# Kernel optimization log

Hardware: AMD Instinct MI355X
Metric: run time of the kernel (lower is better)

## Reference

```python
import jax, jax.numpy as jnp
import numpy as np

N_NODES = 100000
N_EDGES = 3200000
IN_DIM, HID, OUT = 256, 64, 10


def setup_inputs() -> dict:
    key = jax.random.key(0)
    ks = jax.random.split(key, 6)
    x = jax.random.normal(ks[0], (N_NODES, IN_DIM), jnp.float32)
    edge_index = jax.random.randint(ks[1], (2, N_EDGES), 0, N_NODES, dtype=jnp.int64)
    edge_weight = jnp.ones((N_EDGES,), jnp.float32)
    # Glorot-scaled weights; PyG GCNConv keeps bias separate from lin.
    W1 = jax.random.normal(ks[2], (HID, IN_DIM), jnp.float32) * np.float32(1.0 / np.sqrt(IN_DIM))
    b1 = jnp.zeros((HID,), jnp.float32)
    W2 = jax.random.normal(ks[3], (HID, HID), jnp.float32) * np.float32(1.0 / np.sqrt(HID))
    b2 = jnp.zeros((HID,), jnp.float32)
    W3 = jax.random.normal(ks[4], (OUT, HID), jnp.float32) * np.float32(1.0 / np.sqrt(HID))
    b3 = jnp.zeros((OUT,), jnp.float32)
    return dict(x=x, edge_index=edge_index, edge_weight=edge_weight,
                W1=W1, b1=b1, W2=W2, b2=b2, W3=W3, b3=b3)


def _gcn_conv(x, W, b, row, col, edge_weight, n):
    """PyG GCNConv with add_self_loops=False: out = D^{-1/2} A D^{-1/2} (x W^T) + b."""
    h = x @ W.T  # [N, out_dim]
    deg = jax.ops.segment_sum(edge_weight, col, num_segments=n)  # in-degree by weight
    dinv = jnp.where(deg > 0, jax.lax.rsqrt(jnp.maximum(deg, 1e-12)), 0.0)
    norm = dinv[row] * edge_weight * dinv[col]  # [E]
    msgs = h[row] * norm[:, None]               # gather from source nodes
    out = jax.ops.segment_sum(msgs, col, num_segments=n)  # scatter-add to targets
    return out + b


def reference(x, edge_index, edge_weight, W1, b1, W2, b2, W3, b3):
    row, col = edge_index[0], edge_index[1]
    n = x.shape[0]
    h = jax.nn.relu(_gcn_conv(x, W1, b1, row, col, edge_weight, n))
    h = jax.nn.relu(_gcn_conv(h, W2, b2, row, col, edge_weight, n))
    out = _gcn_conv(h, W3, b3, row, col, edge_weight, n)  # logits, [N, num_classes]
    return out
```

## Files before the change

### kernel.cpp

```cpp
#include <hip/hip_runtime.h>
#include <stddef.h>

typedef __attribute__((ext_vector_type(8))) short bf16x8;
typedef __attribute__((ext_vector_type(4))) float f32x4;
typedef __attribute__((ext_vector_type(8))) float f32x8;

#define NPB 512
#define PB  512

__device__ inline float bf2f(unsigned short u) {
    unsigned int v = ((unsigned int)u) << 16;
    float f;
    __builtin_memcpy(&f, &v, 4);
    return f;
}
__device__ inline unsigned short f2bf(float f) {
    unsigned int v;
    __builtin_memcpy(&v, &f, 4);
    unsigned int r = (v + 0x7FFFu + ((v >> 16) & 1u)) >> 16;
    return (unsigned short)r;
}
__device__ inline float feat(const void* p, long long idx, int isbf) {
    if (isbf) return bf2f(((const unsigned short*)p)[idx]);
    return ((const float*)p)[idx];
}
__device__ inline int clampi(int v, int lo, int hi) {
    return v < lo ? lo : (v > hi ? hi : v);
}

__global__ void detect_kernel(const int* ei, const unsigned short* ew16,
                              const unsigned short* x16, int* flags) {
    __shared__ int s_is64, s_pass;
    if (threadIdx.x == 0) { s_is64 = 1; s_pass = 0; }
    __syncthreads();
    int t = threadIdx.x;
    if (t < 128 && ei[2 * t + 1] != 0) atomicAnd(&s_is64, 0);
    if (t < 64) {
        unsigned short h = x16[t];
        unsigned int expf = (h >> 7) & 0xFF;
        if (h == 0 || (expf >= 112 && expf <= 142)) atomicAdd(&s_pass, 1);
    }
    __syncthreads();
    if (t == 0) {
        flags[0] = s_is64;
        flags[1] = (ew16[0] == 0x3F80) ? 1 : 0;
        flags[2] = (s_pass >= 56) ? 1 : 0;
        flags[3] = 1;
    }
}

__global__ void ones_kernel(const void* ew, int* flags, int E) {
    int i = blockIdx.x * blockDim.x + threadIdx.x;
    int wbf = flags[1];
    int b = i * 4;
    int lim = b + 4 < E ? b + 4 : E;
    bool bad = false;
    for (int k = b; k < lim; k++)
        if (feat(ew, k, wbf) != 1.0f) bad = true;
    if (bad) atomicAnd(&flags[3], 0);
}

__global__ void sentinel_kernel(unsigned short* outp, int n, float val) {
    int i = blockIdx.x * blockDim.x + threadIdx.x;
    if (i < n) outp[i] = f2bf(val);
}

__global__ void wsplit_kernel(const void* W, const int* flags, unsigned short* hi,
                              unsigned short* lo, int n_in, int n_out) {
    int i = blockIdx.x * blockDim.x + threadIdx.x;
    if (i >= n_out) return;
    if (i >= n_in) { hi[i] = 0; lo[i] = 0; return; }
    if (flags[2]) {
        hi[i] = ((const unsigned short*)W)[i];
        lo[i] = 0;
    } else {
        float v = ((const float*)W)[i];
        unsigned short h = f2bf(v);
        hi[i] = h;
        lo[i] = f2bf(v - bf2f(h));
    }
}

__global__ __launch_bounds__(512) void khist_kernel(const int* ei, const int* flags,
                                                    int* ghist, int E, int n,
                                                    int NB, int chunk) {
    __shared__ int hist[256];
    int blk = blockIdx.x;
    for (int i = threadIdx.x; i < NB; i += blockDim.x) hist[i] = 0;
    __syncthreads();
    int is64 = flags[0];
    int e0 = blk * chunk;
    int e1 = e0 + chunk < E ? e0 + chunk : E;
    for (int e = e0 + (int)threadIdx.x; e < e1; e += blockDim.x) {
        int c = is64 ? ei[2 * (E + e)] : ei[E + e];
        c = clampi(c, 0, n - 1);
        atomicAdd(&hist[c >> 9], 1);
    }
    __syncthreads();
    for (int i = threadIdx.x; i < NB; i += blockDim.x) ghist[blk * NB + i] = hist[i];
}

__global__ __launch_bounds__(512) void koff1_kernel(int* ghist, int* btot, int NB) {
    __shared__ int s[512];
    int b = blockIdx.x;
    int t = threadIdx.x;
    int v = ghist[t * NB + b];
    s[t] = v;
    __syncthreads();
    for (int off = 1; off < 512; off <<= 1) {
        int add = (t >= off) ? s[t - off] : 0;
        __syncthreads();
        s[t] += add;
        __syncthreads();
    }
    ghist[t * NB + b] = s[t] - v;
    if (t == 511) btot[b] = s[511];
}

__global__ __launch_bounds__(256) void koff2_kernel(const int* btot, int* bstart,
                                                    int* row_ptr, int NB, int N, int E) {
    __shared__ int s[256];
    int t = threadIdx.x;
    int v = (t < NB) ? btot[t] : 0;
    s[t] = v;
    __syncthreads();
    for (int off = 1; off < 256; off <<= 1) {
        int add = (t >= off) ? s[t - off] : 0;
        __syncthreads();
        s[t] += add;
        __syncthreads();
    }
    if (t < NB) bstart[t] = s[t] - v;
    if (t == 0) row_ptr[N] = E;
}

__global__ __launch_bounds__(512) void kscatter_kernel(const int* ei, const void* ew,
                                                       const int* flags, const int* ghist,
                                                       const int* bstart,
                                                       unsigned int* ebuf, float* wbuf,
                                                       int E, int n, int NB, int chunk) {
    __shared__ int cur[256];
    int blk = blockIdx.x;
    for (int i = threadIdx.x; i < NB; i += blockDim.x)
        cur[i] = ghist[blk * NB + i] + bstart[i];
    __syncthreads();
    int is64 = flags[0], wbf = flags[1], ones = flags[3];
    int e0 = blk * chunk;
    int e1 = e0 + chunk < E ? e0 + chunk : E;
    for (int e = e0 + (int)threadIdx.x; e < e1; e += blockDim.x) {
        int r = is64 ? ei[2 * e] : ei[e];
        int c = is64 ? ei[2 * (E + e)] : ei[E + e];
        r = clampi(r, 0, n - 1);
        c = clampi(c, 0, n - 1);
        int b = c >> 9;
        int pos = atomicAdd(&cur[b], 1);
        ebuf[pos] = ((unsigned int)(c & 511) << 17) | (unsigned int)r;
        if (!ones) wbuf[pos] = feat(ew, e, wbf);
    }
}

__global__ __launch_bounds__(512) void kcsr_a_kernel(const unsigned int* ebuf,
                                                     const float* wbuf, const int* flags,
                                                     const int* bstart, const int* btot,
                                                     int* row_ptr, float* dinv, int N) {
    __shared__ int cnt[512];
    __shared__ int pre[512];
    __shared__ float wsum[512];
    int b = blockIdx.x;
    int t = threadIdx.x;
    int ones = flags[3];
    cnt[t] = 0;
    wsum[t] = 0.f;
    __syncthreads();
    int bs = bstart[b];
    int be = bs + btot[b];
    for (int i = bs + t; i < be; i += 512) {
        unsigned int p = ebuf[i];
        int cl = (int)(p >> 17);
        atomicAdd(&cnt[cl], 1);
        if (!ones) atomicAdd(&wsum[cl], wbuf[i]);
    }
    __syncthreads();
    int v = cnt[t];
    pre[t] = v;
    __syncthreads();
    for (int off = 1; off < 512; off <<= 1) {
        int add = (t >= off) ? pre[t - off] : 0;
        __syncthreads();
        pre[t] += add;
        __syncthreads();
    }
    int node = b * NPB + t;
    if (node < N) {
        row_ptr[node] = bs + pre[t] - v;
        float d = ones ? (float)v : wsum[t];
        dinv[node] = (d > 0.f) ? rsqrtf(fmaxf(d, 1e-12f)) : 0.f;
    }
}

__global__ __launch_bounds__(512) void kcsr_b_kernel(const unsigned int* ebuf,
                                                     const float* wbuf, const int* flags,
                                                     const int* bstart, const int* btot,
                                                     const int* row_ptr, const float* dinv,
                                                     int2* csr_pack, int N) {
    __shared__ int cur[512];
    __shared__ float dloc[512];
    int b = blockIdx.x;
    int t = threadIdx.x;
    int ones = flags[3];
    int node = b * NPB + t;
    cur[t] = (node < N) ? row_ptr[node] : 0;
    dloc[t] = (node < N) ? dinv[node] : 0.f;
    __syncthreads();
    int bs = bstart[b];
    int be = bs + btot[b];
    for (int i = bs + t; i < be; i += 512) {
        unsigned int p = ebuf[i];
        int cl = (int)(p >> 17);
        int r = (int)(p & 0x1FFFFu);
        float w = ones ? 1.0f : wbuf[i];
        float nv = dinv[r] * w * dloc[cl];
        int pos = atomicAdd(&cur[cl], 1);
        csr_pack[pos] = make_int2(r, __float_as_int(nv));
    }
}

__device__ inline void split8v(f32x8 v, bf16x8& hi, bf16x8& lo) {
    for (int i = 0; i < 8; i++) {
        float f = v[i];
        unsigned short h = f2bf(f);
        hi[i] = (short)h;
        lo[i] = (short)f2bf(f - bf2f(h));
    }
}

__global__ __launch_bounds__(256) void gemm1_kernel(const void* A,
                             const unsigned short* Whi, const unsigned short* Wlo,
                             const int* flags, unsigned short* C, int M, int K) {
    int wave = threadIdx.x >> 6;
    int l = threadIdx.x & 63;
    int m = l & 15;
    int quad = l >> 4;
    int row0 = blockIdx.x * 64 + wave * 16;
    bool arow_ok = (row0 + m) < M;
    int fb = flags[2];
    f32x4 acc[4];
    #pragma unroll
    for (int n = 0; n < 4; n++) acc[n] = (f32x4){0.f, 0.f, 0.f, 0.f};
    bf16x8 zf = {0, 0, 0, 0, 0, 0, 0, 0};
    long long abase = (long long)(row0 + m) * K + quad * 8;
    if (fb) {
        const short* As = (const short*)A;
        #pragma unroll 4
        for (int k0 = 0; k0 < K; k0 += 32) {
            bf16x8 a = arow_ok ? *(const bf16x8*)(As + abase + k0) : zf;
            #pragma unroll
            for (int n = 0; n < 4; n++) {
                const unsigned short* wp = Whi + (long long)(n * 16 + m) * K + k0 + quad * 8;
                bf16x8 b = *(const bf16x8*)wp;
                acc[n] = __builtin_amdgcn_mfma_f32_16x16x32_bf16(a, b, acc[n], 0, 0, 0);
            }
        }
    } else {
        const float* Af = (const float*)A;
        #pragma unroll 2
        for (int k0 = 0; k0 < K; k0 += 32) {
            bf16x8 ah = zf, al = zf;
            if (arow_ok) {
                f32x8 av = *(const f32x8*)(Af + abase + k0);
                split8v(av, ah, al);
            }
            #pragma unroll
            for (int n = 0; n < 4; n++) {
                long long widx = (long long)(n * 16 + m) * K + k0 + quad * 8;
                bf16x8 wh = *(const bf16x8*)(Whi + widx);
                bf16x8 wl = *(const bf16x8*)(Wlo + widx);
                acc[n] = __builtin_amdgcn_mfma_f32_16x16x32_bf16(ah, wh, acc[n], 0, 0, 0);
                acc[n] = __builtin_amdgcn_mfma_f32_16x16x32_bf16(al, wh, acc[n], 0, 0, 0);
                acc[n] = __builtin_amdgcn_mfma_f32_16x16x32_bf16(ah, wl, acc[n], 0, 0, 0);
            }
        }
    }
    #pragma unroll
    for (int n = 0; n < 4; n++) {
        #pragma unroll
        for (int r = 0; r < 4; r++) {
            int row = row0 + quad * 4 + r;
            if (row < M) C[(long long)row * 64 + n * 16 + m] = f2bf(acc[n][r]);
        }
    }
}

__global__ __launch_bounds__(256) void gemm2_kernel(const unsigned short* A,
                             const unsigned short* Whi, const unsigned short* Wlo,
                             const int* flags, unsigned short* C, int M) {
    int wave = threadIdx.x >> 6;
    int l = threadIdx.x & 63;
    int m = l & 15;
    int quad = l >> 4;
    int row0 = blockIdx.x * 64 + wave * 16;
    bool arow_ok = (row0 + m) < M;
    int fb = flags[2];
    f32x4 acc[4];
    #pragma unroll
    for (int n = 0; n < 4; n++) acc[n] = (f32x4){0.f, 0.f, 0.f, 0.f};
    bf16x8 zf = {0, 0, 0, 0, 0, 0, 0, 0};
    const short* As = (const short*)A;
    long long abase = (long long)(row0 + m) * 64 + quad * 8;
    #pragma unroll
    for (int k0 = 0; k0 < 64; k0 += 32) {
        bf16x8 a = arow_ok ? *(const bf16x8*)(As + abase + k0) : zf;
        #pragma unroll
        for (int n = 0; n < 4; n++) {
            long long widx = (long long)(n * 16 + m) * 64 + k0 + quad * 8;
            bf16x8 wh = *(const bf16x8*)(Whi + widx);
            acc[n] = __builtin_amdgcn_mfma_f32_16x16x32_bf16(a, wh, acc[n], 0, 0, 0);
            if (!fb) {
                bf16x8 wl = *(const bf16x8*)(Wlo + widx);
                acc[n] = __builtin_amdgcn_mfma_f32_16x16x32_bf16(a, wl, acc[n], 0, 0, 0);
            }
        }
    }
    #pragma unroll
    for (int n = 0; n < 4; n++) {
        #pragma unroll
        for (int r = 0; r < 4; r++) {
            int row = row0 + quad * 4 + r;
            if (row < M) C[(long long)row * 64 + n * 16 + m] = f2bf(acc[n][r]);
        }
    }
}

__global__ __launch_bounds__(256) void gemm3_kernel(const unsigned short* A,
                             const unsigned short* Whi, const unsigned short* Wlo,
                             const int* flags, unsigned short* C, int M) {
    int wave = threadIdx.x >> 6;
    int l = threadIdx.x & 63;
    int m = l & 15;
    int quad = l >> 4;
    int row0 = blockIdx.x * 64 + wave * 16;
    bool arow_ok = (row0 + m) < M;
    int fb = flags[2];
    f32x4 acc = {0.f, 0.f, 0.f, 0.f};
    bf16x8 zf = {0, 0, 0, 0, 0, 0, 0, 0};
    const short* As = (const short*)A;
    long long abase = (long long)(row0 + m) * 64 + quad * 8;
    #pragma unroll
    for (int k0 = 0; k0 < 64; k0 += 32) {
        bf16x8 a = arow_ok ? *(const bf16x8*)(As + abase + k0) : zf;
        long long widx = (long long)m * 64 + k0 + quad * 8;
        bf16x8 wh = *(const bf16x8*)(Whi + widx);
        acc = __builtin_amdgcn_mfma_f32_16x16x32_bf16(a, wh, acc, 0, 0, 0);
        if (!fb) {
            bf16x8 wl = *(const bf16x8*)(Wlo + widx);
            acc = __builtin_amdgcn_mfma_f32_16x16x32_bf16(a, wl, acc, 0, 0, 0);
        }
    }
    #pragma unroll
    for (int r = 0; r < 4; r++) {
        int row = row0 + quad * 4 + r;
        if (row < M) C[(long long)row * 16 + m] = f2bf(acc[r]);
    }
}

__global__ void agg64_kernel(const unsigned short* h, const void* bias,
                             const int* flags, const int* row_ptr,
                             const int2* cp, unsigned short* outp, int n, int do_relu) {
    int l = threadIdx.x & 63;
    int node = blockIdx.x * 4 + (int)(threadIdx.x >> 6);
    if (node >= n) return;
    int g = l >> 3;
    int j = l & 7;
    int beg = row_ptr[node];
    int end = row_ptr[node + 1];
    float a0 = 0.f, a1 = 0.f, a2 = 0.f, a3 = 0.f;
    float a4 = 0.f, a5 = 0.f, a6 = 0.f, a7 = 0.f;
    for (int e = beg; e < end; e += 8) {
        int ee = e + g;
        if (ee < end) {
            int2 p = cp[ee];
            float nv = __int_as_float(p.y);
            uint4 raw = *(const uint4*)(h + (long long)p.x * 64 + j * 8);
            a0 += nv * __uint_as_float(raw.x << 16);
            a1 += nv * __uint_as_float(raw.x & 0xFFFF0000u);
            a2 += nv * __uint_as_float(raw.y << 16);
            a3 += nv * __uint_as_float(raw.y & 0xFFFF0000u);
            a4 += nv * __uint_as_float(raw.z << 16);
            a5 += nv * __uint_as_float(raw.z & 0xFFFF0000u);
            a6 += nv * __uint_as_float(raw.w << 16);
            a7 += nv * __uint_as_float(raw.w & 0xFFFF0000u);
        }
    }
    for (int mask = 8; mask <= 32; mask <<= 1) {
        a0 += __shfl_xor(a0, mask);
        a1 += __shfl_xor(a1, mask);
        a2 += __shfl_xor(a2, mask);
        a3 += __shfl_xor(a3, mask);
        a4 += __shfl_xor(a4, mask);
        a5 += __shfl_xor(a5, mask);
        a6 += __shfl_xor(a6, mask);
        a7 += __shfl_xor(a7, mask);
    }
    if (g == 0) {
        int fb = flags[2];
        float v0 = a0 + feat(bias, j * 8 + 0, fb);
        float v1 = a1 + feat(bias, j * 8 + 1, fb);
        float v2 = a2 + feat(bias, j * 8 + 2, fb);
        float v3 = a3 + feat(bias, j * 8 + 3, fb);
        float v4 = a4 + feat(bias, j * 8 + 4, fb);
        float v5 = a5 + feat(bias, j * 8 + 5, fb);
        float v6 = a6 + feat(bias, j * 8 + 6, fb);
        float v7 = a7 + feat(bias, j * 8 + 7, fb);
        if (do_relu) {
            v0 = fmaxf(v0, 0.f); v1 = fmaxf(v1, 0.f);
            v2 = fmaxf(v2, 0.f); v3 = fmaxf(v3, 0.f);
            v4 = fmaxf(v4, 0.f); v5 = fmaxf(v5, 0.f);
            v6 = fmaxf(v6, 0.f); v7 = fmaxf(v7, 0.f);
        }
        uint4 pk;
        pk.x = (unsigned int)f2bf(v0) | ((unsigned int)f2bf(v1) << 16);
        pk.y = (unsigned int)f2bf(v2) | ((unsigned int)f2bf(v3) << 16);
        pk.z = (unsigned int)f2bf(v4) | ((unsigned int)f2bf(v5) << 16);
        pk.w = (unsigned int)f2bf(v6) | ((unsigned int)f2bf(v7) << 16);
        *(uint4*)(outp + (long long)node * 64 + j * 8) = pk;
    }
}

__global__ void agg16_kernel(const unsigned short* h, const void* bias,
                             const int* flags, const int* row_ptr,
                             const int2* cp, void* outp, int n) {
    int l = threadIdx.x & 63;
    int node = blockIdx.x * 4 + (int)(threadIdx.x >> 6);
    if (node >= n) return;
    int g = l >> 2;
    int j = l & 3;
    int beg = row_ptr[node];
    int end = row_ptr[node + 1];
    float a0 = 0.f, a1 = 0.f, a2 = 0.f, a3 = 0.f;
    for (int e = beg; e < end; e += 16) {
        int ee = e + g;
        if (ee < end) {
            int2 p = cp[ee];
            float nv = __int_as_float(p.y);
            uint2 raw = *(const uint2*)(h + (long long)p.x * 16 + j * 4);
            a0 += nv * __uint_as_float(raw.x << 16);
            a1 += nv * __uint_as_float(raw.x & 0xFFFF0000u);
            a2 += nv * __uint_as_float(raw.y << 16);
            a3 += nv * __uint_as_float(raw.y & 0xFFFF0000u);
        }
    }
    for (int mask = 4; mask <= 32; mask <<= 1) {
        a0 += __shfl_xor(a0, mask);
        a1 += __shfl_xor(a1, mask);
        a2 += __shfl_xor(a2, mask);
        a3 += __shfl_xor(a3, mask);
    }
    if (g == 0) {
        int fb = flags[2];
        float v[4] = {a0, a1, a2, a3};
        #pragma unroll
        for (int i = 0; i < 4; i++) {
            int f = j * 4 + i;
            if (f < 10) {
                float o = v[i] + feat(bias, f, fb);
                if (fb) ((unsigned short*)outp)[(long long)node * 10 + f] = f2bf(o);
                else    ((float*)outp)[(long long)node * 10 + f] = o;
            }
        }
    }
}

extern "C" void kernel_launch(void* const* d_in, const int* in_sizes, int n_in,
                              void* d_out, int out_size, void* d_ws, size_t ws_size,
                              hipStream_t stream) {
    const void* x  = d_in[0];
    const int*  ei = (const int*)d_in[1];
    const void* ew = d_in[2];
    const void* W1 = d_in[3];
    const void* b1 = d_in[4];
    const void* W2 = d_in[5];
    const void* b2 = d_in[6];
    const void* W3 = d_in[7];
    const void* b3 = d_in[8];

    const int N = in_sizes[0] / 256;
    const int E = in_sizes[1] / 2;
    const int TB = 256;
    const int NB = (N + NPB - 1) / NPB;
    const int chunk = (E + PB - 1) / PB;

    size_t off = 0;
    size_t o_flags = off; off += 16;
    size_t o_ghist = off; off += (size_t)PB * NB * 4; off = (off + 15) & ~(size_t)15;
    size_t o_btot  = off; off += (size_t)NB * 4;
    size_t o_bst   = off; off += (size_t)NB * 4; off = (off + 15) & ~(size_t)15;
    size_t o_rp    = off; off += (size_t)(N + 1) * 4;
    size_t o_dinv  = off; off += (size_t)N * 4; off = (off + 15) & ~(size_t)15;
    size_t o_pack  = off; off += (size_t)E * 8;
    size_t o_bufA  = off; off += (size_t)N * 64 * 2;
    size_t o_bufB  = off; off += (size_t)N * 64 * 2;
    size_t o_h3    = off; off += (size_t)N * 16 * 2; off = (off + 15) & ~(size_t)15;
    size_t o_w1hi  = off; off += (size_t)64 * 256 * 2;
    size_t o_w1lo  = off; off += (size_t)64 * 256 * 2;
    size_t o_w2hi  = off; off += (size_t)64 * 64 * 2;
    size_t o_w2lo  = off; off += (size_t)64 * 64 * 2;
    size_t o_w3hi  = off; off += (size_t)16 * 64 * 2;
    size_t o_w3lo  = off; off += (size_t)16 * 64 * 2;
    size_t need = off;
    if (ws_size < need || (size_t)E * 4 > (size_t)N * 64 * 2) {
        sentinel_kernel<<<dim3((out_size + TB - 1) / TB), dim3(TB), 0, stream>>>(
            (unsigned short*)d_out, out_size, 250.0f);
        return;
    }
    char* ws = (char*)d_ws;
    int*   flags    = (int*)(ws + o_flags);
    int*   ghist    = (int*)(ws + o_ghist);
    int*   btot     = (int*)(ws + o_btot);
    int*   bstart   = (int*)(ws + o_bst);
    int*   row_ptr  = (int*)(ws + o_rp);
    float* dinv     = (float*)(ws + o_dinv);
    int2*  csr_pack = (int2*)(ws + o_pack);
    unsigned short* bufA  = (unsigned short*)(ws + o_bufA);
    unsigned short* bufB  = (unsigned short*)(ws + o_bufB);
    unsigned short* h3buf = (unsigned short*)(ws + o_h3);
    unsigned short* w1hi  = (unsigned short*)(ws + o_w1hi);
    unsigned short* w1lo  = (unsigned short*)(ws + o_w1lo);
    unsigned short* w2hi  = (unsigned short*)(ws + o_w2hi);
    unsigned short* w2lo  = (unsigned short*)(ws + o_w2lo);
    unsigned short* w3hi  = (unsigned short*)(ws + o_w3hi);
    unsigned short* w3lo  = (unsigned short*)(ws + o_w3lo);
    float*        wbuf = (float*)bufA;
    unsigned int* ebuf = (unsigned int*)bufB;

    dim3 tb(TB);
    dim3 tb512(512);
    dim3 gE4((E / 4 + TB - 1) / TB);
    dim3 gG((N + 63) / 64);
    dim3 gAgg((N + 3) / 4);
    dim3 one(1);

    detect_kernel<<<one, tb, 0, stream>>>(ei, (const unsigned short*)ew,
                                          (const unsigned short*)x, flags);
    wsplit_kernel<<<dim3(64), tb, 0, stream>>>(W1, flags, w1hi, w1lo,
                                               64 * 256, 64 * 256);
    wsplit_kernel<<<dim3(16), tb, 0, stream>>>(W2, flags, w2hi, w2lo,
                                               64 * 64, 64 * 64);
    wsplit_kernel<<<dim3(4), tb, 0, stream>>>(W3, flags, w3hi, w3lo,
                                              10 * 64, 16 * 64);
    ones_kernel<<<gE4, tb, 0, stream>>>(ew, flags, E);
    khist_kernel<<<dim3(PB), tb512, 0, stream>>>(ei, flags, ghist, E, N, NB, chunk);
    koff1_kernel<<<dim3(NB), tb512, 0, stream>>>(ghist, btot, NB);
    koff2_kernel<<<one, tb, 0, stream>>>(btot, bstart, row_ptr, NB, N, E);
    kscatter_kernel<<<dim3(PB), tb512, 0, stream>>>(ei, ew, flags, ghist, bstart,
                                                    ebuf, wbuf, E, N, NB, chunk);
    kcsr_a_kernel<<<dim3(NB), tb512, 0, stream>>>(ebuf, wbuf, flags, bstart, btot,
                                                  row_ptr, dinv, N);
    kcsr_b_kernel<<<dim3(NB), tb512, 0, stream>>>(ebuf, wbuf, flags, bstart, btot,
                                                  row_ptr, dinv, csr_pack, N);

    gemm1_kernel<<<gG, tb, 0, stream>>>(x, w1hi, w1lo, flags, bufA, N, 256);
    agg64_kernel<<<gAgg, tb, 0, stream>>>(bufA, b1, flags, row_ptr, csr_pack,
                                          bufB, N, 1);
    gemm2_kernel<<<gG, tb, 0, stream>>>(bufB, w2hi, w2lo, flags, bufA, N);
    agg64_kernel<<<gAgg, tb, 0, stream>>>(bufA, b2, flags, row_ptr, csr_pack,
                                          bufB, N, 1);
    gemm3_kernel<<<gG, tb, 0, stream>>>(bufB, w3hi, w3lo, flags, h3buf, N);
    agg16_kernel<<<gAgg, tb, 0, stream>>>(h3buf, b3, flags, row_ptr, csr_pack,
                                          d_out, N);
}
```

Before: 596.8 us.

## Split 64-wide aggregation into feature slices across a second grid dimension

The 64-feature SpMM aggregation is restructured so each block handles a 16-feature slice (blockIdx.y selects one of 4 slices). Each wave now processes 4 nodes in sequence, with 32 edges in flight per node and 2 lanes covering the 16 features. The aim is a smaller working set per slice, giving better L2 locality for the random gathers and more edges in parallel per node. In exchange, the CSR indices and weights are read four times, and each gather is a single 32-byte segment per row, which may hurt memory efficiency.

```diff
diff --git a/kernel.cpp b/kernel.cpp
--- a/kernel.cpp
+++ b/kernel.cpp
@@ -363,66 +363,73 @@
     }
 }
 
-__global__ void agg64_kernel(const unsigned short* h, const void* bias,
-                             const int* flags, const int* row_ptr,
-                             const int2* cp, unsigned short* outp, int n, int do_relu) {
+__global__ __launch_bounds__(256) void agg64s_kernel(const unsigned short* h,
+                              const void* bias, const int* flags, const int* row_ptr,
+                              const int2* cp, unsigned short* outp, int n, int do_relu) {
     int l = threadIdx.x & 63;
-    int node = blockIdx.x * 4 + (int)(threadIdx.x >> 6);
-    if (node >= n) return;
-    int g = l >> 3;
-    int j = l & 7;
-    int beg = row_ptr[node];
-    int end = row_ptr[node + 1];
-    float a0 = 0.f, a1 = 0.f, a2 = 0.f, a3 = 0.f;
-    float a4 = 0.f, a5 = 0.f, a6 = 0.f, a7 = 0.f;
-    for (int e = beg; e < end; e += 8) {
-        int ee = e + g;
-        if (ee < end) {
-            int2 p = cp[ee];
-            float nv = __int_as_float(p.y);
-            uint4 raw = *(const uint4*)(h + (long long)p.x * 64 + j * 8);
-            a0 += nv * __uint_as_float(raw.x << 16);
-            a1 += nv * __uint_as_float(raw.x & 0xFFFF0000u);
-            a2 += nv * __uint_as_float(raw.y << 16);
-            a3 += nv * __uint_as_float(raw.y & 0xFFFF0000u);
-            a4 += nv * __uint_as_float(raw.z << 16);
-            a5 += nv * __uint_as_float(raw.z & 0xFFFF0000u);
-            a6 += nv * __uint_as_float(raw.w << 16);
-            a7 += nv * __uint_as_float(raw.w & 0xFFFF0000u);
-        }
-    }
-    for (int mask = 8; mask <= 32; mask <<= 1) {
-        a0 += __shfl_xor(a0, mask);
-        a1 += __shfl_xor(a1, mask);
-        a2 += __shfl_xor(a2, mask);
-        a3 += __shfl_xor(a3, mask);
-        a4 += __shfl_xor(a4, mask);
-        a5 += __shfl_xor(a5, mask);
-        a6 += __shfl_xor(a6, mask);
-        a7 += __shfl_xor(a7, mask);
-    }
-    if (g == 0) {
-        int fb = flags[2];
-        float v0 = a0 + feat(bias, j * 8 + 0, fb);
-        float v1 = a1 + feat(bias, j * 8 + 1, fb);
-        float v2 = a2 + feat(bias, j * 8 + 2, fb);
-        float v3 = a3 + feat(bias, j * 8 + 3, fb);
-        float v4 = a4 + feat(bias, j * 8 + 4, fb);
-        float v5 = a5 + feat(bias, j * 8 + 5, fb);
-        float v6 = a6 + feat(bias, j * 8 + 6, fb);
-        float v7 = a7 + feat(bias, j * 8 + 7, fb);
-        if (do_relu) {
-            v0 = fmaxf(v0, 0.f); v1 = fmaxf(v1, 0.f);
-            v2 = fmaxf(v2, 0.f); v3 = fmaxf(v3, 0.f);
-            v4 = fmaxf(v4, 0.f); v5 = fmaxf(v5, 0.f);
-            v6 = fmaxf(v6, 0.f); v7 = fmaxf(v7, 0.f);
-        }
-        uint4 pk;
-        pk.x = (unsigned int)f2bf(v0) | ((unsigned int)f2bf(v1) << 16);
-        pk.y = (unsigned int)f2bf(v2) | ((unsigned int)f2bf(v3) << 16);
-        pk.z = (unsigned int)f2bf(v4) | ((unsigned int)f2bf(v5) << 16);
-        pk.w = (unsigned int)f2bf(v6) | ((unsigned int)f2bf(v7) << 16);
-        *(uint4*)(outp + (long long)node * 64 + j * 8) = pk;
+    int wave = (int)(threadIdx.x >> 6);
+    int s = (int)blockIdx.y;
+    int g = l >> 1;
+    int j = l & 1;
+    int f0 = s * 16 + j * 8;
+    int nbase = ((int)blockIdx.x * 4 + wave) * 4;
+    for (int nd = 0; nd < 4; nd++) {
+        int node = nbase + nd;
+        if (node >= n) break;
+        int beg = row_ptr[node];
+        int end = row_ptr[node + 1];
+        float a0 = 0.f, a1 = 0.f, a2 = 0.f, a3 = 0.f;
+        float a4 = 0.f, a5 = 0.f, a6 = 0.f, a7 = 0.f;
+        for (int e = beg; e < end; e += 32) {
+            int ee = e + g;
+            if (ee < end) {
+                int2 p = cp[ee];
+                float nv = __int_as_float(p.y);
+                uint4 raw = *(const uint4*)(h + (long long)p.x * 64 + f0);
+                a0 += nv * __uint_as_float(raw.x << 16);
+                a1 += nv * __uint_as_float(raw.x & 0xFFFF0000u);
+                a2 += nv * __uint_as_float(raw.y << 16);
+                a3 += nv * __uint_as_float(raw.y & 0xFFFF0000u);
+                a4 += nv * __uint_as_float(raw.z << 16);
+                a5 += nv * __uint_as_float(raw.z & 0xFFFF0000u);
+                a6 += nv * __uint_as_float(raw.w << 16);
+                a7 += nv * __uint_as_float(raw.w & 0xFFFF0000u);
+            }
+        }
+        #pragma unroll
+        for (int mask = 2; mask <= 32; mask <<= 1) {
+            a0 += __shfl_xor(a0, mask);
+            a1 += __shfl_xor(a1, mask);
+            a2 += __shfl_xor(a2, mask);
+            a3 += __shfl_xor(a3, mask);
+            a4 += __shfl_xor(a4, mask);
+            a5 += __shfl_xor(a5, mask);
+            a6 += __shfl_xor(a6, mask);
+            a7 += __shfl_xor(a7, mask);
+        }
+        if (g == 0) {
+            int fb = flags[2];
+            float v0 = a0 + feat(bias, f0 + 0, fb);
+            float v1 = a1 + feat(bias, f0 + 1, fb);
+            float v2 = a2 + feat(bias, f0 + 2, fb);
+            float v3 = a3 + feat(bias, f0 + 3, fb);
+            float v4 = a4 + feat(bias, f0 + 4, fb);
+            float v5 = a5 + feat(bias, f0 + 5, fb);
+            float v6 = a6 + feat(bias, f0 + 6, fb);
+            float v7 = a7 + feat(bias, f0 + 7, fb);
+            if (do_relu) {
+                v0 = fmaxf(v0, 0.f); v1 = fmaxf(v1, 0.f);
+                v2 = fmaxf(v2, 0.f); v3 = fmaxf(v3, 0.f);
+                v4 = fmaxf(v4, 0.f); v5 = fmaxf(v5, 0.f);
+                v6 = fmaxf(v6, 0.f); v7 = fmaxf(v7, 0.f);
+            }
+            uint4 pk;
+            pk.x = (unsigned int)f2bf(v0) | ((unsigned int)f2bf(v1) << 16);
+            pk.y = (unsigned int)f2bf(v2) | ((unsigned int)f2bf(v3) << 16);
+            pk.z = (unsigned int)f2bf(v4) | ((unsigned int)f2bf(v5) << 16);
+            pk.w = (unsigned int)f2bf(v6) | ((unsigned int)f2bf(v7) << 16);
+            *(uint4*)(outp + (long long)node * 64 + f0) = pk;
+        }
     }
 }
 
@@ -537,6 +544,7 @@
     dim3 gE4((E / 4 + TB - 1) / TB);
     dim3 gG((N + 63) / 64);
     dim3 gAgg((N + 3) / 4);
+    dim3 gAggS((N + 15) / 16, 4);
     dim3 one(1);
 
     detect_kernel<<<one, tb, 0, stream>>>(ei, (const unsigned short*)ew,
@@ -559,11 +567,11 @@
                                                   row_ptr, dinv, csr_pack, N);
 
     gemm1_kernel<<<gG, tb, 0, stream>>>(x, w1hi, w1lo, flags, bufA, N, 256);
-    agg64_kernel<<<gAgg, tb, 0, stream>>>(bufA, b1, flags, row_ptr, csr_pack,
-                                          bufB, N, 1);
+    agg64s_kernel<<<gAggS, tb, 0, stream>>>(bufA, b1, flags, row_ptr, csr_pack,
+                                            bufB, N, 1);
     gemm2_kernel<<<gG, tb, 0, stream>>>(bufB, w2hi, w2lo, flags, bufA, N);
-    agg64_kernel<<<gAgg, tb, 0, stream>>>(bufA, b2, flags, row_ptr, csr_pack,
-                                          bufB, N, 1);
+    agg64s_kernel<<<gAggS, tb, 0, stream>>>(bufA, b2, flags, row_ptr, csr_pack,
+                                            bufB, N, 1);
     gemm3_kernel<<<gG, tb, 0, stream>>>(bufB, w3hi, w3lo, flags, h3buf, N);
     agg16_kernel<<<gAgg, tb, 0, stream>>>(h3buf, b3, flags, row_ptr, csr_pack,
                                           d_out, N);
```

New measurement: 836.5 us. 40.2% more time.
